# Kernel optimization log

Measured on AMD Instinct MI355X. Metric: run time of the kernel, lower is better.

The kernel has to match this reference:

```python
import jax, jax.numpy as jnp
import numpy as np

N = 10000      # nodes
DEG = 32       # avg degree
D_IN = 256     # in_feats
H = 128        # hidden_layers[0] == hidden_layers[2]
K = 3          # hidden_layers[1] = Chebyshev order
D_OUT = 64     # out_feat


def setup_inputs() -> dict:
    key = jax.random.key(0)
    ks = jax.random.split(key, 8)
    x = jax.random.normal(ks[0], (N, D_IN), jnp.float32)
    # sparse binary adjacency built by scattering into a dense [N, N] matrix
    src = jax.random.randint(ks[1], (N * DEG,), 0, N)
    dst = jax.random.randint(ks[2], (N * DEG,), 0, N)
    adj = jnp.zeros((N, N), jnp.float32).at[src, dst].set(1.0)
    init = lambda k, shape, fan: jax.random.normal(k, shape, jnp.float32) / np.sqrt(fan)
    W_in = init(ks[3], (D_IN, H), D_IN)
    b_in = jnp.zeros((H,), jnp.float32)
    W_cheb = init(ks[4], (K * H, H), K * H)   # dgl ChebConv: Linear(k*in, out)
    b_cheb = jnp.zeros((H,), jnp.float32)
    W_out = init(ks[5], (H, D_OUT), H)
    b_out = jnp.zeros((D_OUT,), jnp.float32)
    return dict(x=x, adj=adj, W_in=W_in, b_in=b_in, W_cheb=W_cheb,
                b_cheb=b_cheb, W_out=W_out, b_out=b_out)


def reference(x, adj, W_in, b_in, W_cheb, b_cheb, W_out, b_out):
    n = x.shape[0]
    # graph construction from dense adjacency (eager, like adj.to_dense().nonzero())
    src, dst = jnp.nonzero(adj)
    # symmetric normalization on in-degrees (dgl ChebConv, norm clamped at 1)
    deg = jax.ops.segment_sum(jnp.ones(src.shape[0], jnp.float32), dst, num_segments=n)
    norm = jnp.clip(deg, 1.0) ** -0.5  # [n]
    re_norm = 2.0 / 2.0  # lambda_max = [2] -> re_norm = 1

    def prop(h):
        # D^{-1/2} A D^{-1/2} h : gather at src, scatter-add at dst
        return jax.ops.segment_sum((h * norm[:, None])[src], dst, num_segments=n) * norm[:, None]

    # input linear + relu
    h = jax.nn.relu(x @ W_in + b_in)
    # Chebyshev recursion (dgl ChebConv with lambda_max=2)
    X0 = h
    X1 = -re_norm * prop(X0) + (re_norm - 1.0) * X0
    Xs = [X0, X1]
    Xpp, Xp = X0, X1
    for _ in range(2, K):
        Xi = -2.0 * re_norm * prop(Xp) + 2.0 * (re_norm - 1.0) * Xp - Xpp
        Xs.append(Xi)
        Xpp, Xp = Xp, Xi
    hc = jax.nn.relu(jnp.concatenate(Xs, axis=1) @ W_cheb + b_cheb)  # [n, H]
    return hc @ W_out + b_out  # [n, D_OUT]
```

## Files before the change

### kernel.cpp

```cpp
#include <hip/hip_runtime.h>
#include <hip/hip_bf16.h>
#include <cstdint>
#include <cstddef>

#define NN 10000
#define MAXDEG 128
#define LDX 384

__device__ __forceinline__ float bf2f(unsigned short u) {
    unsigned int x = ((unsigned int)u) << 16;
    union { unsigned int i; float f; } c; c.i = x; return c.f;
}
__device__ __forceinline__ unsigned short f2bf(float f) {
    union { float f; unsigned int i; } c; c.f = f;
    unsigned int x = c.i;
    return (unsigned short)((x + 0x7fffu + ((x >> 16) & 1u)) >> 16);
}

__global__ __launch_bounds__(256) void zero_cnt(int* __restrict__ cnt) {
    int i = blockIdx.x * 256 + threadIdx.x;
    if (i < NN) cnt[i] = 0;
}

__global__ __launch_bounds__(256) void adj_scan(const float4* __restrict__ adj4,
                                                int total4,
                                                int* __restrict__ cnt,
                                                int* __restrict__ csr) {
    int idx = blockIdx.x * blockDim.x + threadIdx.x;
    int stride = gridDim.x * blockDim.x;
    for (int p = idx; p < total4; p += stride) {
        float4 v = adj4[p];
        if (v.x != 0.f || v.y != 0.f || v.z != 0.f || v.w != 0.f) {
            int lin = p * 4;
            #pragma unroll
            for (int c = 0; c < 4; ++c) {
                float f = (c == 0) ? v.x : (c == 1) ? v.y : (c == 2) ? v.z : v.w;
                if (f != 0.f) {
                    int l = lin + c;
                    int i = l / NN;
                    int j = l - i * NN;
                    int pos = atomicAdd(&cnt[j], 1);
                    if (pos < MAXDEG) csr[j * MAXDEG + pos] = i;
                }
            }
        }
    }
}

template<bool SUB>
__global__ __launch_bounds__(256) void prop_k(unsigned short* __restrict__ X,
                                              const int* __restrict__ csr,
                                              const int* __restrict__ cnt,
                                              int srcOff, int dstOff, float scale) {
    int j = blockIdx.x * 4 + (threadIdx.x >> 6);
    if (j >= NN) return;
    int lane = threadIdx.x & 63;
    int cj = cnt[j];
    int cn = min(cj, MAXDEG);
    const int* nb = csr + j * MAXDEG;
    float ax = 0.f, ay = 0.f;
    for (int e = 0; e < cn; ++e) {
        int i = nb[e];
        float w = rsqrtf(fmaxf((float)cnt[i], 1.f));
        uint32_t h2 = *(const uint32_t*)(X + (size_t)i * LDX + srcOff + lane * 2);
        ax = fmaf(w, bf2f((unsigned short)h2), ax);
        ay = fmaf(w, bf2f((unsigned short)(h2 >> 16)), ay);
    }
    float s = scale * rsqrtf(fmaxf((float)cj, 1.f));
    float rx = s * ax, ry = s * ay;
    if (SUB) {
        uint32_t x0 = *(const uint32_t*)(X + (size_t)j * LDX + lane * 2);
        rx -= bf2f((unsigned short)x0);
        ry -= bf2f((unsigned short)(x0 >> 16));
    }
    uint32_t o = (uint32_t)f2bf(rx) | ((uint32_t)f2bf(ry) << 16);
    *(uint32_t*)(X + (size_t)j * LDX + dstOff + lane * 2) = o;
}

__global__ __launch_bounds__(256) void gemm_in(const float* __restrict__ A,
                                               const float* __restrict__ W,
                                               const float* __restrict__ bias,
                                               unsigned short* __restrict__ Xc,
                                               int M) {
    constexpr int K = 256, N = 128, BM = 32, KC = 128;
    constexpr int COLS2 = N / 2, GR = 256 / COLS2, RPG = BM / GR;
    __shared__ float Wl[KC * N];
    __shared__ float Al[BM * KC];
    int t = threadIdx.x;
    int r0 = blockIdx.x * BM;
    int c2 = t % COLS2;
    int g = t / COLS2;

    float2 acc[RPG];
    #pragma unroll
    for (int i = 0; i < RPG; ++i) acc[i] = make_float2(0.f, 0.f);

    for (int kk = 0; kk < K; kk += KC) {
        __syncthreads();
        #pragma unroll
        for (int i = 0; i < KC * N / 4 / 256; ++i) {
            int idx = t + i * 256;
            ((float4*)Wl)[idx] = ((const float4*)(W + (size_t)kk * N))[idx];
        }
        #pragma unroll
        for (int i = 0; i < BM * KC / 4 / 256; ++i) {
            int idx = t + i * 256;
            int row = idx / (KC / 4);
            int cf = idx % (KC / 4);
            float4 v = make_float4(0.f, 0.f, 0.f, 0.f);
            if (r0 + row < M)
                v = *(const float4*)(A + (size_t)(r0 + row) * K + kk + cf * 4);
            *(float4*)(Al + row * KC + cf * 4) = v;
        }
        __syncthreads();
        for (int k = 0; k < KC; k += 4) {
            float4 av[RPG];
            #pragma unroll
            for (int rr = 0; rr < RPG; ++rr)
                av[rr] = *(const float4*)(Al + (g * RPG + rr) * KC + k);
            #pragma unroll
            for (int k2 = 0; k2 < 4; ++k2) {
                float2 wv = *(const float2*)(Wl + (k + k2) * N + c2 * 2);
                #pragma unroll
                for (int rr = 0; rr < RPG; ++rr) {
                    float a = (k2 == 0) ? av[rr].x : (k2 == 1) ? av[rr].y
                              : (k2 == 2) ? av[rr].z : av[rr].w;
                    acc[rr].x = fmaf(a, wv.x, acc[rr].x);
                    acc[rr].y = fmaf(a, wv.y, acc[rr].y);
                }
            }
        }
    }
    float2 bv = *(const float2*)(bias + c2 * 2);
    #pragma unroll
    for (int rr = 0; rr < RPG; ++rr) {
        int r = r0 + g * RPG + rr;
        if (r < M) {
            float vx = fmaxf(acc[rr].x + bv.x, 0.f);
            float vy = fmaxf(acc[rr].y + bv.y, 0.f);
            uint32_t o = (uint32_t)f2bf(vx) | ((uint32_t)f2bf(vy) << 16);
            *(uint32_t*)(Xc + (size_t)r * LDX + c2 * 2) = o;
        }
    }
}

__global__ __launch_bounds__(256) void gemm_cheb_out(
        const unsigned short* __restrict__ A,
        const float* __restrict__ Wc,
        const float* __restrict__ bc,
        const float* __restrict__ Wo,
        const float* __restrict__ bo,
        float* __restrict__ out,
        int M) {
    constexpr int K = 384, N = 128, BM = 32, KC = 128;
    constexpr int COLS2 = N / 2, GR = 256 / COLS2, RPG = BM / GR;
    __shared__ float smem[KC * N + BM * KC];
    float* Wl = smem;
    float* Al = smem + KC * N;
    int t = threadIdx.x;
    int r0 = blockIdx.x * BM;
    int c2 = t % COLS2;
    int g = t / COLS2;

    float2 acc[RPG];
    #pragma unroll
    for (int i = 0; i < RPG; ++i) acc[i] = make_float2(0.f, 0.f);

    for (int kk = 0; kk < K; kk += KC) {
        __syncthreads();
        #pragma unroll
        for (int i = 0; i < KC * N / 4 / 256; ++i) {
            int idx = t + i * 256;
            ((float4*)Wl)[idx] = ((const float4*)(Wc + (size_t)kk * N))[idx];
        }
        #pragma unroll
        for (int i = 0; i < BM * KC / 4 / 256; ++i) {
            int eidx = (t + i * 256) * 4;
            int row = eidx / KC;
            int col = eidx % KC;
            float4 v = make_float4(0.f, 0.f, 0.f, 0.f);
            if (r0 + row < M) {
                uint2 u = *(const uint2*)(A + (size_t)(r0 + row) * LDX + kk + col);
                v.x = bf2f((unsigned short)u.x);
                v.y = bf2f((unsigned short)(u.x >> 16));
                v.z = bf2f((unsigned short)u.y);
                v.w = bf2f((unsigned short)(u.y >> 16));
            }
            *(float4*)(Al + row * KC + col) = v;
        }
        __syncthreads();
        for (int k = 0; k < KC; k += 4) {
            float4 av[RPG];
            #pragma unroll
            for (int rr = 0; rr < RPG; ++rr)
                av[rr] = *(const float4*)(Al + (g * RPG + rr) * KC + k);
            #pragma unroll
            for (int k2 = 0; k2 < 4; ++k2) {
                float2 wv = *(const float2*)(Wl + (k + k2) * N + c2 * 2);
                #pragma unroll
                for (int rr = 0; rr < RPG; ++rr) {
                    float a = (k2 == 0) ? av[rr].x : (k2 == 1) ? av[rr].y
                              : (k2 == 2) ? av[rr].z : av[rr].w;
                    acc[rr].x = fmaf(a, wv.x, acc[rr].x);
                    acc[rr].y = fmaf(a, wv.y, acc[rr].y);
                }
            }
        }
    }

    __syncthreads();
    float* hcL  = smem;
    float* WoL  = smem + BM * N;
    float2 bv = *(const float2*)(bc + c2 * 2);
    #pragma unroll
    for (int rr = 0; rr < RPG; ++rr) {
        int row = g * RPG + rr;
        float vx = fmaxf(acc[rr].x + bv.x, 0.f);
        float vy = fmaxf(acc[rr].y + bv.y, 0.f);
        *(float2*)(hcL + row * N + c2 * 2) = make_float2(vx, vy);
    }
    #pragma unroll
    for (int i = 0; i < 128 * 64 / 4 / 256; ++i) {
        int idx = t + i * 256;
        ((float4*)WoL)[idx] = ((const float4*)Wo)[idx];
    }
    __syncthreads();

    int c32 = t & 31;
    int g2 = t >> 5;
    float2 a2[4];
    #pragma unroll
    for (int i = 0; i < 4; ++i) a2[i] = make_float2(0.f, 0.f);
    for (int k = 0; k < 128; k += 4) {
        float4 hv[4];
        #pragma unroll
        for (int rr = 0; rr < 4; ++rr)
            hv[rr] = *(const float4*)(hcL + (g2 * 4 + rr) * N + k);
        #pragma unroll
        for (int k2 = 0; k2 < 4; ++k2) {
            float2 wv = *(const float2*)(WoL + (k + k2) * 64 + c32 * 2);
            #pragma unroll
            for (int rr = 0; rr < 4; ++rr) {
                float a = (k2 == 0) ? hv[rr].x : (k2 == 1) ? hv[rr].y
                          : (k2 == 2) ? hv[rr].z : hv[rr].w;
                a2[rr].x = fmaf(a, wv.x, a2[rr].x);
                a2[rr].y = fmaf(a, wv.y, a2[rr].y);
            }
        }
    }
    float2 bov = *(const float2*)(bo + c32 * 2);
    #pragma unroll
    for (int rr = 0; rr < 4; ++rr) {
        int r = r0 + g2 * 4 + rr;
        if (r < M) {
            float2 v = make_float2(a2[rr].x + bov.x, a2[rr].y + bov.y);
            *(float2*)(out + (size_t)r * 64 + c32 * 2) = v;
        }
    }
}

extern "C" void kernel_launch(void* const* d_in, const int* in_sizes, int n_in,
                              void* d_out, int out_size, void* d_ws, size_t ws_size,
                              hipStream_t stream) {
    const float* x      = (const float*)d_in[0];
    const float* adj    = (const float*)d_in[1];
    const float* W_in   = (const float*)d_in[2];
    const float* b_in   = (const float*)d_in[3];
    const float* W_cheb = (const float*)d_in[4];
    const float* b_cheb = (const float*)d_in[5];
    const float* W_out  = (const float*)d_in[6];
    const float* b_out  = (const float*)d_in[7];
    float* out = (float*)d_out;

    char* ws = (char*)d_ws;
    int*            cnt = (int*)(ws + 0);
    int*            csr = (int*)(ws + 40960);
    unsigned short* Xc  = (unsigned short*)(ws + 5160960);

    int adj_total = in_sizes[1];

    zero_cnt<<<(NN + 255) / 256, 256, 0, stream>>>(cnt);
    adj_scan<<<4096, 256, 0, stream>>>((const float4*)adj, adj_total / 4, cnt, csr);
    gemm_in<<<(NN + 31) / 32, 256, 0, stream>>>(x, W_in, b_in, Xc, NN);
    prop_k<false><<<(NN + 3) / 4, 256, 0, stream>>>(Xc, csr, cnt, 0, 128, -1.0f);
    prop_k<true><<<(NN + 3) / 4, 256, 0, stream>>>(Xc, csr, cnt, 128, 256, -2.0f);
    gemm_cheb_out<<<(NN + 31) / 32, 256, 0, stream>>>(Xc, W_cheb, b_cheb, W_out, b_out, out, NN);
}
```

Baseline: 270.3 us.

## Fuse adjacency scan with input GEMM, and use bf16 MFMA for Cheb/output GEMMs

Merges the adjacency scan, the input GEMM and a weight-transpose/bf16 conversion into one heterogeneous kernel so the GEMM blocks overlap with the memory-bound scan. The Chebyshev and output GEMMs are rewritten to use bf16 MFMA instructions with pre-transposed bf16 weights, replacing the fp32 FMA loops. The propagation loop is unrolled by two with separate accumulators to raise memory-level parallelism, and the zeroing kernel is replaced by a memset. Weight rounding to bf16 adds precision loss, and the single conversion block could become a tail straggler.

```diff
diff --git a/kernel.cpp b/kernel.cpp
--- a/kernel.cpp
+++ b/kernel.cpp
@@ -7,9 +7,16 @@
 #define MAXDEG 128
 #define LDX 384
 
+#define GEMM_BLKS 313
+#define CONV_BLK  1
+#define SCAN_BLKS 3072
+#define FAT_BLKS  (GEMM_BLKS + CONV_BLK + SCAN_BLKS)
+
+typedef __attribute__((ext_vector_type(8))) short bf16x8;
+typedef __attribute__((ext_vector_type(4))) float f32x4;
+
 __device__ __forceinline__ float bf2f(unsigned short u) {
-    unsigned int x = ((unsigned int)u) << 16;
-    union { unsigned int i; float f; } c; c.i = x; return c.f;
+    union { unsigned int i; float f; } c; c.i = ((unsigned int)u) << 16; return c.f;
 }
 __device__ __forceinline__ unsigned short f2bf(float f) {
     union { float f; unsigned int i; } c; c.f = f;
@@ -17,30 +24,103 @@
     return (unsigned short)((x + 0x7fffu + ((x >> 16) & 1u)) >> 16);
 }
 
-__global__ __launch_bounds__(256) void zero_cnt(int* __restrict__ cnt) {
-    int i = blockIdx.x * 256 + threadIdx.x;
-    if (i < NN) cnt[i] = 0;
-}
-
-__global__ __launch_bounds__(256) void adj_scan(const float4* __restrict__ adj4,
-                                                int total4,
-                                                int* __restrict__ cnt,
-                                                int* __restrict__ csr) {
-    int idx = blockIdx.x * blockDim.x + threadIdx.x;
-    int stride = gridDim.x * blockDim.x;
-    for (int p = idx; p < total4; p += stride) {
-        float4 v = adj4[p];
-        if (v.x != 0.f || v.y != 0.f || v.z != 0.f || v.w != 0.f) {
-            int lin = p * 4;
-            #pragma unroll
-            for (int c = 0; c < 4; ++c) {
-                float f = (c == 0) ? v.x : (c == 1) ? v.y : (c == 2) ? v.z : v.w;
-                if (f != 0.f) {
-                    int l = lin + c;
-                    int i = l / NN;
-                    int j = l - i * NN;
-                    int pos = atomicAdd(&cnt[j], 1);
-                    if (pos < MAXDEG) csr[j * MAXDEG + pos] = i;
+__global__ __launch_bounds__(256) void fat_scan_gemm(
+        const float4* __restrict__ adj4, int total4,
+        int* __restrict__ cnt, int* __restrict__ csr,
+        const float* __restrict__ x, const float* __restrict__ W_in,
+        const float* __restrict__ b_in,
+        const float* __restrict__ W_cheb, const float* __restrict__ W_out,
+        unsigned short* __restrict__ Xc,
+        unsigned short* __restrict__ Wtc, unsigned short* __restrict__ Wto) {
+    __shared__ float smem[10240];
+    int bid = blockIdx.x;
+    int t = threadIdx.x;
+
+    if (bid < GEMM_BLKS) {
+        constexpr int K = 256, N = 128, BM = 32, KC = 64;
+        float* Wl = smem;
+        float* Al = smem + KC * N;
+        int r0 = bid * BM;
+        int c2 = t & 63;
+        int g  = t >> 6;
+        float2 acc[8];
+        #pragma unroll
+        for (int i = 0; i < 8; ++i) acc[i] = make_float2(0.f, 0.f);
+
+        for (int kk = 0; kk < K; kk += KC) {
+            __syncthreads();
+            #pragma unroll
+            for (int i = 0; i < KC * N / 4 / 256; ++i) {
+                int idx = t + i * 256;
+                ((float4*)Wl)[idx] = ((const float4*)(W_in + (size_t)kk * N))[idx];
+            }
+            #pragma unroll
+            for (int i = 0; i < BM * KC / 4 / 256; ++i) {
+                int idx = t + i * 256;
+                int row = idx >> 4;
+                int cf  = idx & 15;
+                float4 v = make_float4(0.f, 0.f, 0.f, 0.f);
+                if (r0 + row < NN)
+                    v = *(const float4*)(x + (size_t)(r0 + row) * K + kk + cf * 4);
+                *(float4*)(Al + row * KC + cf * 4) = v;
+            }
+            __syncthreads();
+            for (int k = 0; k < KC; k += 4) {
+                float4 av[8];
+                #pragma unroll
+                for (int rr = 0; rr < 8; ++rr)
+                    av[rr] = *(const float4*)(Al + (g * 8 + rr) * KC + k);
+                #pragma unroll
+                for (int k2 = 0; k2 < 4; ++k2) {
+                    float2 wv = *(const float2*)(Wl + (k + k2) * N + c2 * 2);
+                    #pragma unroll
+                    for (int rr = 0; rr < 8; ++rr) {
+                        float a = (k2 == 0) ? av[rr].x : (k2 == 1) ? av[rr].y
+                                  : (k2 == 2) ? av[rr].z : av[rr].w;
+                        acc[rr].x = fmaf(a, wv.x, acc[rr].x);
+                        acc[rr].y = fmaf(a, wv.y, acc[rr].y);
+                    }
+                }
+            }
+        }
+        float2 bv = *(const float2*)(b_in + c2 * 2);
+        #pragma unroll
+        for (int rr = 0; rr < 8; ++rr) {
+            int r = r0 + g * 8 + rr;
+            if (r < NN) {
+                float vx = fmaxf(acc[rr].x + bv.x, 0.f);
+                float vy = fmaxf(acc[rr].y + bv.y, 0.f);
+                uint32_t o = (uint32_t)f2bf(vx) | ((uint32_t)f2bf(vy) << 16);
+                *(uint32_t*)(Xc + (size_t)r * LDX + c2 * 2) = o;
+            }
+        }
+    } else if (bid == GEMM_BLKS) {
+        for (int idx = t; idx < 384 * 128; idx += 256) {
+            int k = idx >> 7, c = idx & 127;
+            Wtc[c * 384 + k] = f2bf(W_cheb[idx]);
+        }
+        for (int idx = t; idx < 128 * 64; idx += 256) {
+            int k = idx >> 6, c = idx & 63;
+            Wto[c * 128 + k] = f2bf(W_out[idx]);
+        }
+    } else {
+        int sid = bid - (GEMM_BLKS + CONV_BLK);
+        int idx = sid * 256 + t;
+        int stride = SCAN_BLKS * 256;
+        for (int p = idx; p < total4; p += stride) {
+            float4 v = adj4[p];
+            if (v.x != 0.f || v.y != 0.f || v.z != 0.f || v.w != 0.f) {
+                int lin = p * 4;
+                #pragma unroll
+                for (int c = 0; c < 4; ++c) {
+                    float f = (c == 0) ? v.x : (c == 1) ? v.y : (c == 2) ? v.z : v.w;
+                    if (f != 0.f) {
+                        int l = lin + c;
+                        int i = l / NN;
+                        int j = l - i * NN;
+                        int pos = atomicAdd(&cnt[j], 1);
+                        if (pos < MAXDEG) csr[j * MAXDEG + pos] = i;
+                    }
                 }
             }
         }
@@ -58,16 +138,29 @@
     int cj = cnt[j];
     int cn = min(cj, MAXDEG);
     const int* nb = csr + j * MAXDEG;
-    float ax = 0.f, ay = 0.f;
-    for (int e = 0; e < cn; ++e) {
-        int i = nb[e];
-        float w = rsqrtf(fmaxf((float)cnt[i], 1.f));
-        uint32_t h2 = *(const uint32_t*)(X + (size_t)i * LDX + srcOff + lane * 2);
-        ax = fmaf(w, bf2f((unsigned short)h2), ax);
-        ay = fmaf(w, bf2f((unsigned short)(h2 >> 16)), ay);
+    float ax0 = 0.f, ay0 = 0.f, ax1 = 0.f, ay1 = 0.f;
+    int e = 0;
+    for (; e + 2 <= cn; e += 2) {
+        int i0 = nb[e], i1 = nb[e + 1];
+        int c0 = cnt[i0], c1 = cnt[i1];
+        uint32_t h0 = *(const uint32_t*)(X + (size_t)i0 * LDX + srcOff + lane * 2);
+        uint32_t h1 = *(const uint32_t*)(X + (size_t)i1 * LDX + srcOff + lane * 2);
+        float w0 = rsqrtf(fmaxf((float)c0, 1.f));
+        float w1 = rsqrtf(fmaxf((float)c1, 1.f));
+        ax0 = fmaf(w0, bf2f((unsigned short)h0), ax0);
+        ay0 = fmaf(w0, bf2f((unsigned short)(h0 >> 16)), ay0);
+        ax1 = fmaf(w1, bf2f((unsigned short)h1), ax1);
+        ay1 = fmaf(w1, bf2f((unsigned short)(h1 >> 16)), ay1);
+    }
+    if (e < cn) {
+        int i0 = nb[e];
+        float w0 = rsqrtf(fmaxf((float)cnt[i0], 1.f));
+        uint32_t h0 = *(const uint32_t*)(X + (size_t)i0 * LDX + srcOff + lane * 2);
+        ax0 = fmaf(w0, bf2f((unsigned short)h0), ax0);
+        ay0 = fmaf(w0, bf2f((unsigned short)(h0 >> 16)), ay0);
     }
     float s = scale * rsqrtf(fmaxf((float)cj, 1.f));
-    float rx = s * ax, ry = s * ay;
+    float rx = s * (ax0 + ax1), ry = s * (ay0 + ay1);
     if (SUB) {
         uint32_t x0 = *(const uint32_t*)(X + (size_t)j * LDX + lane * 2);
         rx -= bf2f((unsigned short)x0);
@@ -77,184 +170,73 @@
     *(uint32_t*)(X + (size_t)j * LDX + dstOff + lane * 2) = o;
 }
 
-__global__ __launch_bounds__(256) void gemm_in(const float* __restrict__ A,
-                                               const float* __restrict__ W,
-                                               const float* __restrict__ bias,
-                                               unsigned short* __restrict__ Xc,
-                                               int M) {
-    constexpr int K = 256, N = 128, BM = 32, KC = 128;
-    constexpr int COLS2 = N / 2, GR = 256 / COLS2, RPG = BM / GR;
-    __shared__ float Wl[KC * N];
-    __shared__ float Al[BM * KC];
+__global__ __launch_bounds__(256) void cheb_out_mfma(
+        const unsigned short* __restrict__ Xc,
+        const unsigned short* __restrict__ Wtc,
+        const float* __restrict__ bc,
+        const unsigned short* __restrict__ Wto,
+        const float* __restrict__ bo,
+        float* __restrict__ out) {
+    __shared__ unsigned short hcL[32][136];
     int t = threadIdx.x;
-    int r0 = blockIdx.x * BM;
-    int c2 = t % COLS2;
-    int g = t / COLS2;
-
-    float2 acc[RPG];
+    int w = t >> 6, lane = t & 63;
+    int r0 = blockIdx.x * 32;
+    int lr = lane & 15;
+    int kg = lane >> 4;
+
+    f32x4 acc[2][2] = {};
+    for (int k0 = 0; k0 < 384; k0 += 32) {
+        bf16x8 a[2], b[2];
+        #pragma unroll
+        for (int m = 0; m < 2; ++m) {
+            int row = r0 + m * 16 + lr;
+            row = min(row, NN - 1);
+            a[m] = *(const bf16x8*)(Xc + (size_t)row * LDX + k0 + kg * 8);
+        }
+        #pragma unroll
+        for (int n = 0; n < 2; ++n) {
+            int col = w * 32 + n * 16 + lr;
+            b[n] = *(const bf16x8*)(Wtc + (size_t)col * 384 + k0 + kg * 8);
+        }
+        #pragma unroll
+        for (int m = 0; m < 2; ++m)
+            #pragma unroll
+            for (int n = 0; n < 2; ++n)
+                acc[m][n] = __builtin_amdgcn_mfma_f32_16x16x32_bf16(a[m], b[n], acc[m][n], 0, 0, 0);
+    }
     #pragma unroll
-    for (int i = 0; i < RPG; ++i) acc[i] = make_float2(0.f, 0.f);
-
-    for (int kk = 0; kk < K; kk += KC) {
-        __syncthreads();
-        #pragma unroll
-        for (int i = 0; i < KC * N / 4 / 256; ++i) {
-            int idx = t + i * 256;
-            ((float4*)Wl)[idx] = ((const float4*)(W + (size_t)kk * N))[idx];
-        }
-        #pragma unroll
-        for (int i = 0; i < BM * KC / 4 / 256; ++i) {
-            int idx = t + i * 256;
-            int row = idx / (KC / 4);
-            int cf = idx % (KC / 4);
-            float4 v = make_float4(0.f, 0.f, 0.f, 0.f);
-            if (r0 + row < M)
-                v = *(const float4*)(A + (size_t)(r0 + row) * K + kk + cf * 4);
-            *(float4*)(Al + row * KC + cf * 4) = v;
-        }
-        __syncthreads();
-        for (int k = 0; k < KC; k += 4) {
-            float4 av[RPG];
-            #pragma unroll
-            for (int rr = 0; rr < RPG; ++rr)
-                av[rr] = *(const float4*)(Al + (g * RPG + rr) * KC + k);
-            #pragma unroll
-            for (int k2 = 0; k2 < 4; ++k2) {
-                float2 wv = *(const float2*)(Wl + (k + k2) * N + c2 * 2);
-                #pragma unroll
-                for (int rr = 0; rr < RPG; ++rr) {
-                    float a = (k2 == 0) ? av[rr].x : (k2 == 1) ? av[rr].y
-                              : (k2 == 2) ? av[rr].z : av[rr].w;
-                    acc[rr].x = fmaf(a, wv.x, acc[rr].x);
-                    acc[rr].y = fmaf(a, wv.y, acc[rr].y);
-                }
-            }
-        }
-    }
-    float2 bv = *(const float2*)(bias + c2 * 2);
+    for (int m = 0; m < 2; ++m) {
+        #pragma unroll
+        for (int n = 0; n < 2; ++n) {
+            int col = w * 32 + n * 16 + lr;
+            float bv = bc[col];
+            #pragma unroll
+            for (int r = 0; r < 4; ++r) {
+                int row = m * 16 + kg * 4 + r;
+                hcL[row][col] = f2bf(fmaxf(acc[m][n][r] + bv, 0.f));
+            }
+        }
+    }
+    __syncthreads();
+    int rt = w >> 1, ch = w & 1;
+    f32x4 a2[2] = {};
+    for (int k0 = 0; k0 < 128; k0 += 32) {
+        bf16x8 af = *(const bf16x8*)(&hcL[rt * 16 + lr][k0 + kg * 8]);
+        #pragma unroll
+        for (int n = 0; n < 2; ++n) {
+            int col = ch * 32 + n * 16 + lr;
+            bf16x8 bf_ = *(const bf16x8*)(Wto + (size_t)col * 128 + k0 + kg * 8);
+            a2[n] = __builtin_amdgcn_mfma_f32_16x16x32_bf16(af, bf_, a2[n], 0, 0, 0);
+        }
+    }
     #pragma unroll
-    for (int rr = 0; rr < RPG; ++rr) {
-        int r = r0 + g * RPG + rr;
-        if (r < M) {
-            float vx = fmaxf(acc[rr].x + bv.x, 0.f);
-            float vy = fmaxf(acc[rr].y + bv.y, 0.f);
-            uint32_t o = (uint32_t)f2bf(vx) | ((uint32_t)f2bf(vy) << 16);
-            *(uint32_t*)(Xc + (size_t)r * LDX + c2 * 2) = o;
-        }
-    }
-}
-
-__global__ __launch_bounds__(256) void gemm_cheb_out(
-        const unsigned short* __restrict__ A,
-        const float* __restrict__ Wc,
-        const float* __restrict__ bc,
-        const float* __restrict__ Wo,
-        const float* __restrict__ bo,
-        float* __restrict__ out,
-        int M) {
-    constexpr int K = 384, N = 128, BM = 32, KC = 128;
-    constexpr int COLS2 = N / 2, GR = 256 / COLS2, RPG = BM / GR;
-    __shared__ float smem[KC * N + BM * KC];
-    float* Wl = smem;
-    float* Al = smem + KC * N;
-    int t = threadIdx.x;
-    int r0 = blockIdx.x * BM;
-    int c2 = t % COLS2;
-    int g = t / COLS2;
-
-    float2 acc[RPG];
-    #pragma unroll
-    for (int i = 0; i < RPG; ++i) acc[i] = make_float2(0.f, 0.f);
-
-    for (int kk = 0; kk < K; kk += KC) {
-        __syncthreads();
-        #pragma unroll
-        for (int i = 0; i < KC * N / 4 / 256; ++i) {
-            int idx = t + i * 256;
-            ((float4*)Wl)[idx] = ((const float4*)(Wc + (size_t)kk * N))[idx];
-        }
-        #pragma unroll
-        for (int i = 0; i < BM * KC / 4 / 256; ++i) {
-            int eidx = (t + i * 256) * 4;
-            int row = eidx / KC;
-            int col = eidx % KC;
-            float4 v = make_float4(0.f, 0.f, 0.f, 0.f);
-            if (r0 + row < M) {
-                uint2 u = *(const uint2*)(A + (size_t)(r0 + row) * LDX + kk + col);
-                v.x = bf2f((unsigned short)u.x);
-                v.y = bf2f((unsigned short)(u.x >> 16));
-                v.z = bf2f((unsigned short)u.y);
-                v.w = bf2f((unsigned short)(u.y >> 16));
-            }
-            *(float4*)(Al + row * KC + col) = v;
-        }
-        __syncthreads();
-        for (int k = 0; k < KC; k += 4) {
-            float4 av[RPG];
-            #pragma unroll
-            for (int rr = 0; rr < RPG; ++rr)
-                av[rr] = *(const float4*)(Al + (g * RPG + rr) * KC + k);
-            #pragma unroll
-            for (int k2 = 0; k2 < 4; ++k2) {
-                float2 wv = *(const float2*)(Wl + (k + k2) * N + c2 * 2);
-                #pragma unroll
-                for (int rr = 0; rr < RPG; ++rr) {
-                    float a = (k2 == 0) ? av[rr].x : (k2 == 1) ? av[rr].y
-                              : (k2 == 2) ? av[rr].z : av[rr].w;
-                    acc[rr].x = fmaf(a, wv.x, acc[rr].x);
-                    acc[rr].y = fmaf(a, wv.y, acc[rr].y);
-                }
-            }
-        }
-    }
-
-    __syncthreads();
-    float* hcL  = smem;
-    float* WoL  = smem + BM * N;
-    float2 bv = *(const float2*)(bc + c2 * 2);
-    #pragma unroll
-    for (int rr = 0; rr < RPG; ++rr) {
-        int row = g * RPG + rr;
-        float vx = fmaxf(acc[rr].x + bv.x, 0.f);
-        float vy = fmaxf(acc[rr].y + bv.y, 0.f);
-        *(float2*)(hcL + row * N + c2 * 2) = make_float2(vx, vy);
-    }
-    #pragma unroll
-    for (int i = 0; i < 128 * 64 / 4 / 256; ++i) {
-        int idx = t + i * 256;
-        ((float4*)WoL)[idx] = ((const float4*)Wo)[idx];
-    }
-    __syncthreads();
-
-    int c32 = t & 31;
-    int g2 = t >> 5;
-    float2 a2[4];
-    #pragma unroll
-    for (int i = 0; i < 4; ++i) a2[i] = make_float2(0.f, 0.f);
-    for (int k = 0; k < 128; k += 4) {
-        float4 hv[4];
-        #pragma unroll
-        for (int rr = 0; rr < 4; ++rr)
-            hv[rr] = *(const float4*)(hcL + (g2 * 4 + rr) * N + k);
-        #pragma unroll
-        for (int k2 = 0; k2 < 4; ++k2) {
-            float2 wv = *(const float2*)(WoL + (k + k2) * 64 + c32 * 2);
-            #pragma unroll
-            for (int rr = 0; rr < 4; ++rr) {
-                float a = (k2 == 0) ? hv[rr].x : (k2 == 1) ? hv[rr].y
-                          : (k2 == 2) ? hv[rr].z : hv[rr].w;
-                a2[rr].x = fmaf(a, wv.x, a2[rr].x);
-                a2[rr].y = fmaf(a, wv.y, a2[rr].y);
-            }
-        }
-    }
-    float2 bov = *(const float2*)(bo + c32 * 2);
-    #pragma unroll
-    for (int rr = 0; rr < 4; ++rr) {
-        int r = r0 + g2 * 4 + rr;
-        if (r < M) {
-            float2 v = make_float2(a2[rr].x + bov.x, a2[rr].y + bov.y);
-            *(float2*)(out + (size_t)r * 64 + c32 * 2) = v;
+    for (int n = 0; n < 2; ++n) {
+        int col = ch * 32 + n * 16 + lr;
+        float bv = bo[col];
+        #pragma unroll
+        for (int r = 0; r < 4; ++r) {
+            int row = r0 + rt * 16 + kg * 4 + r;
+            if (row < NN) out[(size_t)row * 64 + col] = a2[n][r] + bv;
         }
     }
 }
@@ -276,13 +258,16 @@
     int*            cnt = (int*)(ws + 0);
     int*            csr = (int*)(ws + 40960);
     unsigned short* Xc  = (unsigned short*)(ws + 5160960);
+    unsigned short* Wtc = (unsigned short*)(ws + 12845056);
+    unsigned short* Wto = (unsigned short*)(ws + 12943360);
 
     int adj_total = in_sizes[1];
 
-    zero_cnt<<<(NN + 255) / 256, 256, 0, stream>>>(cnt);
-    adj_scan<<<4096, 256, 0, stream>>>((const float4*)adj, adj_total / 4, cnt, csr);
-    gemm_in<<<(NN + 31) / 32, 256, 0, stream>>>(x, W_in, b_in, Xc, NN);
+    hipMemsetAsync(cnt, 0, NN * sizeof(int), stream);
+    fat_scan_gemm<<<FAT_BLKS, 256, 0, stream>>>(
+        (const float4*)adj, adj_total / 4, cnt, csr,
+        x, W_in, b_in, W_cheb, W_out, Xc, Wtc, Wto);
     prop_k<false><<<(NN + 3) / 4, 256, 0, stream>>>(Xc, csr, cnt, 0, 128, -1.0f);
     prop_k<true><<<(NN + 3) / 4, 256, 0, stream>>>(Xc, csr, cnt, 128, 256, -2.0f);
-    gemm_cheb_out<<<(NN + 31) / 32, 256, 0, stream>>>(Xc, W_cheb, b_cheb, W_out, b_out, out, NN);
-}
+    cheb_out_mfma<<<(NN + 31) / 32, 256, 0, stream>>>(Xc, Wtc, b_cheb, Wto, b_out, out);
+}
```

Result: faster. 238.5 us (-11.8%).
